# Optimization experiments

Hardware: AMD Instinct MI355X
Metric: run time of the kernel (lower is better)

## Reference

```python
import jax, jax.numpy as jnp
import numpy as np

D_MODEL = 2048
NHEAD = 16
HEAD_DIM = D_MODEL // NHEAD  # 128
B, S = 2, 2048
THETA = 10000.0


def setup_inputs() -> dict:
    key = jax.random.key(0)
    ks = jax.random.split(key, 10)
    sc = 1.0 / np.sqrt(D_MODEL)
    inp = {
        "x": jax.random.normal(ks[0], (B, S, D_MODEL), dtype=jnp.float32),
        "mask": jnp.tril(jnp.ones((1, 1, S, S), dtype=jnp.int32)),
        "Wq": jax.random.normal(ks[1], (D_MODEL, D_MODEL), dtype=jnp.float32) * sc,
        "bq": jax.random.normal(ks[2], (D_MODEL,), dtype=jnp.float32) * 0.01,
        "Wk": jax.random.normal(ks[3], (D_MODEL, D_MODEL), dtype=jnp.float32) * sc,
        "bk": jax.random.normal(ks[4], (D_MODEL,), dtype=jnp.float32) * 0.01,
        "Wv": jax.random.normal(ks[5], (D_MODEL, D_MODEL), dtype=jnp.float32) * sc,
        "bv": jax.random.normal(ks[6], (D_MODEL,), dtype=jnp.float32) * 0.01,
        "Wo": jax.random.normal(ks[7], (D_MODEL, D_MODEL), dtype=jnp.float32) * sc,
        "bo": jax.random.normal(ks[8], (D_MODEL,), dtype=jnp.float32) * 0.01,
    }
    return inp


def _rope(x):
    # x: [B, H, S, D]; rotary applied to first D/2 dims (per the torch module's chunk(2)).
    D = x.shape[-1]
    half = D // 2            # rotary slice size (64)
    quarter = half // 2      # rotate_half split (32)
    seq = x.shape[2]
    inv_freq = 1.0 / (THETA ** (jnp.arange(0, D, 2, dtype=jnp.float32) / D))  # [D/2]
    t = jnp.arange(seq, dtype=jnp.float32)
    freqs = jnp.einsum("i,j->ij", t, inv_freq)  # [S, D/2]
    # emb = cat(freqs, freqs) then sliced to [:half] == freqs[:, :half]
    cos = jnp.cos(freqs)[None, None, :, :half]  # [1,1,S,half]
    sin = jnp.sin(freqs)[None, None, :, :half]
    x_rope, x_pass = x[..., :half], x[..., half:]
    x1, x2 = x_rope[..., :quarter], x_rope[..., quarter:]
    rotated = jnp.concatenate([-x2, x1], axis=-1)
    x_rope = x_rope * cos + rotated * sin
    return jnp.concatenate([x_rope, x_pass], axis=-1)


def reference(x, mask, Wq, bq, Wk, bk, Wv, bv, Wo, bo):
    b, s, _ = x.shape
    def proj(W, bias):
        y = jnp.einsum("bsd,ed->bse", x, W) + bias  # torch Linear: x @ W.T + b
        return y.reshape(b, s, NHEAD, HEAD_DIM).transpose(0, 2, 1, 3)  # [B,H,S,Dh]
    q = _rope(proj(Wq, bq))
    k = _rope(proj(Wk, bk))
    v = proj(Wv, bv)
    scores = jnp.einsum("bhqd,bhkd->bhqk", q, k) / jnp.sqrt(jnp.float32(HEAD_DIM))
    scores = jnp.where(mask == 0, jnp.float32(-1e9), scores)
    a = jax.nn.softmax(scores, axis=-1)
    o = jnp.einsum("bhqk,bhkd->bhqd", a, v)
    o = o.transpose(0, 2, 1, 3).reshape(b, s, D_MODEL)
    return jnp.einsum("bsd,ed->bse", o, Wo) + bo
```

## Files before the change

kernel.cpp:

```cpp
#include <hip/hip_runtime.h>
#include <stdint.h>
#include <math.h>

typedef short short8 __attribute__((ext_vector_type(8)));
typedef float f32x4 __attribute__((ext_vector_type(4)));

#define S_LEN   2048
#define DMODEL  2048
#define NHEADS  16
#define HDIM    128
#define NBATCH  2
#define BHTOT   32
#define MROWS   4096

#define XB_OFF   ((size_t)0)
#define WQ_OFF   ((size_t)16777216)
#define WK_OFF   ((size_t)25165824)
#define WV_OFF   ((size_t)33554432)
#define Q_OFF    ((size_t)41943040)
#define K_OFF    ((size_t)58720256)
#define VT_OFF   ((size_t)75497472)
#define COS_OFF  ((size_t)92274688)
#define SIN_OFF  ((size_t)92798976)

__device__ __forceinline__ unsigned short f2bf(float f) {
  unsigned int u = __float_as_uint(f);
  unsigned int r = (u + 0x7FFFu + ((u >> 16) & 1u)) >> 16;
  return (unsigned short)r;
}
__device__ __forceinline__ float bf2f(unsigned short b) {
  return __uint_as_float(((unsigned int)b) << 16);
}

__device__ __forceinline__ void gl_lds16(const unsigned short* g, unsigned short* l) {
  __builtin_amdgcn_global_load_lds(
      (const __attribute__((address_space(1))) unsigned int*)(g),
      (__attribute__((address_space(3))) unsigned int*)(l),
      16, 0, 0);
}

__global__ __launch_bounds__(256) void k_cvt(const float* __restrict__ src,
                                             unsigned short* __restrict__ dst, int n4) {
  int i = blockIdx.x * 256 + threadIdx.x;
  if (i >= n4) return;
  float4 v = ((const float4*)src)[i];
  ushort4 o;
  o.x = f2bf(v.x); o.y = f2bf(v.y); o.z = f2bf(v.z); o.w = f2bf(v.w);
  ((ushort4*)dst)[i] = o;
}

__global__ __launch_bounds__(256) void k_prep(
    const float* __restrict__ x, const float* __restrict__ Wq,
    const float* __restrict__ Wk, const float* __restrict__ Wv,
    unsigned short* __restrict__ xb, unsigned short* __restrict__ wqb,
    unsigned short* __restrict__ wkb, unsigned short* __restrict__ wvb,
    float* __restrict__ ct, float* __restrict__ st) {
  int i = blockIdx.x * 256 + threadIdx.x;
  if (i < 5242880) {
    const float* s; unsigned short* d; int off;
    if (i < 2097152) { s = x; d = xb; off = i; }
    else {
      int j = i - 2097152, sel = j >> 20;
      off = j & 1048575;
      s = (sel == 0) ? Wq : (sel == 1 ? Wk : Wv);
      d = (sel == 0) ? wqb : (sel == 1 ? wkb : wvb);
    }
    float4 v = ((const float4*)s)[off];
    ushort4 o;
    o.x = f2bf(v.x); o.y = f2bf(v.y); o.z = f2bf(v.z); o.w = f2bf(v.w);
    ((ushort4*)d)[off] = o;
  } else {
    int j = i - 5242880;
    if (j < S_LEN * 64) {
      int s = j >> 6, jj = j & 63;
      float inv = expf(-(float)(2 * jj) * (9.210340371976184f / 128.0f));
      float ang = (float)s * inv;
      ct[j] = cosf(ang);
      st[j] = sinf(ang);
    }
  }
}

#define CP 136
__global__ __launch_bounds__(256) void k_gemm_qkv(
    const unsigned short* __restrict__ xb,
    const unsigned short* __restrict__ wqb, const unsigned short* __restrict__ wkb,
    const unsigned short* __restrict__ wvb,
    const float* __restrict__ bq, const float* __restrict__ bk, const float* __restrict__ bv,
    const float* __restrict__ ct, const float* __restrict__ st,
    unsigned short* __restrict__ qr, unsigned short* __restrict__ kr,
    unsigned short* __restrict__ vt) {
  __shared__ unsigned short SMEM[128 * CP];
  unsigned short* As = SMEM;
  unsigned short* Bs = SMEM + 8192;
  int bid = blockIdx.y * 32 + blockIdx.x;
  int nb = (bid & 7) * 192 + (bid >> 3);
  int m0 = (nb & 31) * 128;
  int n0g = (nb >> 5) * 128;
  int wsel = n0g >> 11;
  int nw0 = n0g & (DMODEL - 1);
  const unsigned short* W = (wsel == 0) ? wqb : (wsel == 1 ? wkb : wvb);
  const float* bias = (wsel == 0) ? bq : (wsel == 1 ? bk : bv);
  int tid = threadIdx.x, lane = tid & 63, wid = tid >> 6;
  int wr = wid >> 1, wc = wid & 1;
  int lq = lane & 15, lk = lane >> 4;
  int gr = wid * 32 + (lane >> 3);
  int gc = ((lane & 7) * 8) ^ ((lane >> 3) << 3);

  f32x4 acc[4][4];
#pragma unroll
  for (int m = 0; m < 4; m++)
#pragma unroll
    for (int n = 0; n < 4; n++) { acc[m][n][0]=0.f; acc[m][n][1]=0.f; acc[m][n][2]=0.f; acc[m][n][3]=0.f; }

  for (int k0 = 0; k0 < DMODEL; k0 += 64) {
#pragma unroll
    for (int i = 0; i < 4; i++) {
      gl_lds16(xb + (size_t)(m0 + gr + i * 8) * DMODEL + k0 + gc, As + (wid * 32 + i * 8) * 64);
      gl_lds16(W  + (size_t)(nw0 + gr + i * 8) * DMODEL + k0 + gc, Bs + (wid * 32 + i * 8) * 64);
    }
    __syncthreads();
#pragma unroll
    for (int kk = 0; kk < 2; kk++) {
      short8 af[4], bfr[4];
      int sw = (lq & 7) << 3;
#pragma unroll
      for (int m = 0; m < 4; m++)
        af[m] = *(const short8*)&As[(wr * 64 + m * 16 + lq) * 64 + ((kk * 32 + lk * 8) ^ sw)];
#pragma unroll
      for (int n = 0; n < 4; n++)
        bfr[n] = *(const short8*)&Bs[(wc * 64 + n * 16 + lq) * 64 + ((kk * 32 + lk * 8) ^ sw)];
#pragma unroll
      for (int m = 0; m < 4; m++)
#pragma unroll
        for (int n = 0; n < 4; n++)
          acc[m][n] = __builtin_amdgcn_mfma_f32_16x16x32_bf16(af[m], bfr[n], acc[m][n], 0, 0, 0);
    }
    __syncthreads();
  }

  int h = nw0 >> 7, b = m0 >> 11, s0 = m0 & (S_LEN - 1);
  float bi[4];
#pragma unroll
  for (int n = 0; n < 4; n++) bi[n] = bias[nw0 + wc * 64 + n * 16 + lq];

  if (wsel < 2) {
    float qs = (wsel == 0) ? 0.08838834764831843f : 1.0f;
    if (wc == 0) {
#pragma unroll
      for (int m = 0; m < 4; m++) {
        int sl = wr * 64 + m * 16 + lk * 4;
#pragma unroll
        for (int r = 0; r < 4; r++) {
          int s = (s0 + sl + r);
          const float* cb = ct + s * 64;
          const float* sb = st + s * 64;
#pragma unroll
          for (int n = 0; n < 2; n++) {
            int fq = n * 16 + lq;
            float x1 = acc[m][n][r] + bi[n];
            float x2 = acc[m][n + 2][r] + bi[n + 2];
            SMEM[(sl + r) * CP + fq]      = f2bf((x1 * cb[fq]      - x2 * sb[fq])      * qs);
            SMEM[(sl + r) * CP + fq + 32] = f2bf((x2 * cb[fq + 32] + x1 * sb[fq + 32]) * qs);
          }
        }
      }
    } else {
#pragma unroll
      for (int m = 0; m < 4; m++) {
        int sl = wr * 64 + m * 16 + lk * 4;
#pragma unroll
        for (int n = 0; n < 4; n++) {
          int fq = 64 + n * 16 + lq;
#pragma unroll
          for (int r = 0; r < 4; r++)
            SMEM[(sl + r) * CP + fq] = f2bf((acc[m][n][r] + bi[n]) * qs);
        }
      }
    }
    __syncthreads();
    int row = tid >> 1, hf2 = tid & 1;
    unsigned short* dstb = (wsel == 0 ? qr : kr) +
        ((size_t)(b * NHEADS + h) * S_LEN + s0 + row) * HDIM + hf2 * 64;
    const unsigned short* srcb = &SMEM[row * CP + hf2 * 64];
#pragma unroll
    for (int j = 0; j < 8; j++)
      *(short8*)(dstb + j * 8) = *(const short8*)(srcb + j * 8);
  } else {
#pragma unroll
    for (int m = 0; m < 4; m++) {
      int sl = wr * 64 + m * 16 + lk * 4;
#pragma unroll
      for (int n = 0; n < 4; n++) {
        int fq = wc * 64 + n * 16 + lq;
#pragma unroll
        for (int r = 0; r < 4; r++)
          SMEM[fq * CP + sl + r] = f2bf(acc[m][n][r] + bi[n]);
      }
    }
    __syncthreads();
    int row = tid >> 1, hf2 = tid & 1;
    unsigned short* dstb = vt +
        ((size_t)(b * NHEADS + h) * HDIM + row) * S_LEN + s0 + hf2 * 64;
    const unsigned short* srcb = &SMEM[row * CP + hf2 * 64];
#pragma unroll
    for (int j = 0; j < 8; j++)
      *(short8*)(dstb + j * 8) = *(const short8*)(srcb + j * 8);
  }
}

__device__ __forceinline__ void attn_sm_pv(
    f32x4* sacc, f32x4* acco, float* rm, float* rs,
    unsigned short (*Psw)[72], const unsigned short* V0,
    int lq, int lk, int rsw) {
  float mx4[4];
  int need = 0;
#pragma unroll
  for (int r = 0; r < 4; r++) {
    float mx = fmaxf(fmaxf(sacc[0][r], sacc[1][r]), fmaxf(sacc[2][r], sacc[3][r]));
    mx = fmaxf(mx, __shfl_xor(mx, 1, 64));
    mx = fmaxf(mx, __shfl_xor(mx, 2, 64));
    mx = fmaxf(mx, __shfl_xor(mx, 4, 64));
    mx = fmaxf(mx, __shfl_xor(mx, 8, 64));
    mx4[r] = mx;
    need |= (mx - rm[r] > 8.0f) ? 1 : 0;
  }
  if (__any(need)) {
#pragma unroll
    for (int r = 0; r < 4; r++) {
      float mnew = fmaxf(rm[r], mx4[r]);
      float corr = __expf(rm[r] - mnew);
      rs[r] *= corr;
#pragma unroll
      for (int nd = 0; nd < 8; nd++) acco[nd][r] *= corr;
      rm[r] = mnew;
    }
  }
#pragma unroll
  for (int r = 0; r < 4; r++) {
    float psum = 0.f;
#pragma unroll
    for (int n = 0; n < 4; n++) {
      float p = __expf(sacc[n][r] - rm[r]);
      sacc[n][r] = p;
      psum += p;
    }
    psum += __shfl_xor(psum, 1, 64);
    psum += __shfl_xor(psum, 2, 64);
    psum += __shfl_xor(psum, 4, 64);
    psum += __shfl_xor(psum, 8, 64);
    rs[r] += psum;
  }
#pragma unroll
  for (int n = 0; n < 4; n++)
#pragma unroll
    for (int r = 0; r < 4; r++)
      Psw[lk * 4 + r][n * 16 + lq] = f2bf(sacc[n][r]);
#pragma unroll
  for (int ks2 = 0; ks2 < 2; ks2++) {
    short8 pa = *(const short8*)&Psw[lq][ks2 * 32 + lk * 8];
#pragma unroll
    for (int nd = 0; nd < 8; nd++) {
      short8 vf = *(const short8*)&V0[(nd * 16 + lq) * 64 + ((ks2 * 32 + lk * 8) ^ rsw)];
      acco[nd] = __builtin_amdgcn_mfma_f32_16x16x32_bf16(pa, vf, acco[nd], 0, 0, 0);
    }
  }
}

__global__ __launch_bounds__(256, 2) void k_attn(
    const unsigned short* __restrict__ qr, const unsigned short* __restrict__ kr,
    const unsigned short* __restrict__ vt, unsigned short* __restrict__ ob) {
  __shared__ unsigned short Kl[2][64 * 128];
  __shared__ unsigned short Vl[2][128 * 64];
  __shared__ unsigned short Ps[4][16][72];
  int bh = blockIdx.x;
  int yy = blockIdx.y;
  int f = (yy < 8) ? yy : 23 - yy;
  int qtA = 31 - f, qtB = f;
  int q0A = qtA * 64, q0B = qtB * 64;
  int b = bh >> 4, h = bh & 15;
  int tid = threadIdx.x, lane = tid & 63, w = tid >> 6;
  int lq = lane & 15, lk = lane >> 4;
  const unsigned short* kbh = kr + (size_t)bh * S_LEN * HDIM;
  const unsigned short* vbh = vt + (size_t)bh * HDIM * S_LEN;
  int ksrow = tid >> 4;
  int kscol = ((tid & 15) * 8) ^ ((ksrow & 7) << 3);
  int vsrow = tid >> 3;
  int vscol = ((tid & 7) * 8) ^ ((vsrow & 7) << 3);
  int ldso = tid * 8;
  int rsw = (lq & 7) << 3;

  const unsigned short* qbA =
      qr + ((size_t)bh * S_LEN + q0A + w * 16 + lq) * HDIM + lk * 8;
  const unsigned short* qbB =
      qr + ((size_t)bh * S_LEN + q0B + w * 16 + lq) * HDIM + lk * 8;
  short8 qfA[4], qfB[4];
#pragma unroll
  for (int ks = 0; ks < 4; ks++) {
    qfA[ks] = *(const short8*)(qbA + ks * 32);
    qfB[ks] = *(const short8*)(qbB + ks * 32);
  }

  f32x4 accoA[8], accoB[8];
#pragma unroll
  for (int nd = 0; nd < 8; nd++) {
    accoA[nd][0]=0.f; accoA[nd][1]=0.f; accoA[nd][2]=0.f; accoA[nd][3]=0.f;
    accoB[nd][0]=0.f; accoB[nd][1]=0.f; accoB[nd][2]=0.f; accoB[nd][3]=0.f;
  }
  float rmA[4], rsA[4], rmB[4], rsB[4];
#pragma unroll
  for (int r = 0; r < 4; r++) { rmA[r] = -3.0e38f; rsA[r] = 0.f; rmB[r] = -3.0e38f; rsB[r] = 0.f; }

#pragma unroll
  for (int c = 0; c < 4; c++) {
    gl_lds16(kbh + (size_t)(c * 16 + ksrow) * HDIM + kscol, &Kl[0][c * 2048 + ldso]);
    gl_lds16(vbh + (size_t)(c * 32 + vsrow) * S_LEN + vscol, &Vl[0][c * 2048 + ldso]);
  }
  __syncthreads();
  int cur = 0;

  for (int t = 0; t <= qtA; t++) {
    int kv0 = t * 64;
    if (t < qtA) {
      int nx = kv0 + 64;
#pragma unroll
      for (int c = 0; c < 4; c++) {
        gl_lds16(kbh + (size_t)(nx + c * 16 + ksrow) * HDIM + kscol,
                 &Kl[cur ^ 1][c * 2048 + ldso]);
        gl_lds16(vbh + (size_t)(c * 32 + vsrow) * S_LEN + nx + vscol,
                 &Vl[cur ^ 1][c * 2048 + ldso]);
      }
    }
    const unsigned short* K0 = &Kl[cur][0];
    const unsigned short* V0 = &Vl[cur][0];
    bool actB = (t <= qtB);

    f32x4 saccA[4], saccB[4];
#pragma unroll
    for (int n = 0; n < 4; n++) {
      saccA[n][0]=0.f; saccA[n][1]=0.f; saccA[n][2]=0.f; saccA[n][3]=0.f;
      saccB[n][0]=0.f; saccB[n][1]=0.f; saccB[n][2]=0.f; saccB[n][3]=0.f;
    }
    if (actB) {
#pragma unroll
      for (int ks = 0; ks < 4; ks++)
#pragma unroll
        for (int n = 0; n < 4; n++) {
          short8 kf = *(const short8*)&K0[(n * 16 + lq) * 128 + ((ks * 32 + lk * 8) ^ rsw)];
          saccA[n] = __builtin_amdgcn_mfma_f32_16x16x32_bf16(qfA[ks], kf, saccA[n], 0, 0, 0);
          saccB[n] = __builtin_amdgcn_mfma_f32_16x16x32_bf16(qfB[ks], kf, saccB[n], 0, 0, 0);
        }
    } else {
#pragma unroll
      for (int ks = 0; ks < 4; ks++)
#pragma unroll
        for (int n = 0; n < 4; n++) {
          short8 kf = *(const short8*)&K0[(n * 16 + lq) * 128 + ((ks * 32 + lk * 8) ^ rsw)];
          saccA[n] = __builtin_amdgcn_mfma_f32_16x16x32_bf16(qfA[ks], kf, saccA[n], 0, 0, 0);
        }
    }
    if (t == qtA) {
#pragma unroll
      for (int n = 0; n < 4; n++)
#pragma unroll
        for (int r = 0; r < 4; r++) {
          int qrow = q0A + w * 16 + lk * 4 + r;
          int kvc = kv0 + n * 16 + lq;
          if (kvc > qrow) saccA[n][r] = -3.0e38f;
        }
    }
    attn_sm_pv(saccA, accoA, rmA, rsA, Ps[w], V0, lq, lk, rsw);
    if (actB) {
      if (t == qtB) {
#pragma unroll
        for (int n = 0; n < 4; n++)
#pragma unroll
          for (int r = 0; r < 4; r++) {
            int qrow = q0B + w * 16 + lk * 4 + r;
            int kvc = kv0 + n * 16 + lq;
            if (kvc > qrow) saccB[n][r] = -3.0e38f;
          }
      }
      attn_sm_pv(saccB, accoB, rmB, rsB, Ps[w], V0, lq, lk, rsw);
    }
    __syncthreads();
    cur ^= 1;
  }

#pragma unroll
  for (int r = 0; r < 4; r++) {
    float invA = 1.0f / rsA[r];
    int srowA = q0A + w * 16 + lk * 4 + r;
    unsigned short* dstA = ob + ((size_t)b * S_LEN + srowA) * DMODEL + h * HDIM;
#pragma unroll
    for (int nd = 0; nd < 8; nd++) dstA[nd * 16 + lq] = f2bf(accoA[nd][r] * invA);
    float invB = 1.0f / rsB[r];
    int srowB = q0B + w * 16 + lk * 4 + r;
    unsigned short* dstB = ob + ((size_t)b * S_LEN + srowB) * DMODEL + h * HDIM;
#pragma unroll
    for (int nd = 0; nd < 8; nd++) dstB[nd * 16 + lq] = f2bf(accoB[nd][r] * invB);
  }
}

__global__ __launch_bounds__(256) void k_gemm_out(
    const unsigned short* __restrict__ ob, const unsigned short* __restrict__ wob,
    const float* __restrict__ bo, float* __restrict__ out) {
  __shared__ unsigned short As[128][64];
  __shared__ unsigned short Bs[128][64];
  int bid = blockIdx.y * 32 + blockIdx.x;
  int nb = (bid & 7) * 64 + (bid >> 3);
  int m0 = (nb & 31) * 128;
  int n0 = (nb >> 5) * 128;
  int tid = threadIdx.x, lane = tid & 63, wid = tid >> 6;
  int wr = wid >> 1, wc = wid & 1;
  int lq = lane & 15, lk = lane >> 4;
  int gr = wid * 32 + (lane >> 3);
  int gc = ((lane & 7) * 8) ^ ((lane >> 3) << 3);

  f32x4 acc[4][4];
#pragma unroll
  for (int m = 0; m < 4; m++)
#pragma unroll
    for (int n = 0; n < 4; n++) { acc[m][n][0]=0.f; acc[m][n][1]=0.f; acc[m][n][2]=0.f; acc[m][n][3]=0.f; }

  for (int k0 = 0; k0 < DMODEL; k0 += 64) {
#pragma unroll
    for (int i = 0; i < 4; i++) {
      gl_lds16(ob  + (size_t)(m0 + gr + i * 8) * DMODEL + k0 + gc, &As[wid * 32 + i * 8][0]);
      gl_lds16(wob + (size_t)(n0 + gr + i * 8) * DMODEL + k0 + gc, &Bs[wid * 32 + i * 8][0]);
    }
    __syncthreads();
#pragma unroll
    for (int kk = 0; kk < 2; kk++) {
      short8 af[4], bfr[4];
      int sw = (lq & 7) << 3;
#pragma unroll
      for (int m = 0; m < 4; m++)
        af[m] = *(const short8*)&As[wr * 64 + m * 16 + lq][(kk * 32 + lk * 8) ^ sw];
#pragma unroll
      for (int n = 0; n < 4; n++)
        bfr[n] = *(const short8*)&Bs[wc * 64 + n * 16 + lq][(kk * 32 + lk * 8) ^ sw];
#pragma unroll
      for (int m = 0; m < 4; m++)
#pragma unroll
        for (int n = 0; n < 4; n++)
          acc[m][n] = __builtin_amdgcn_mfma_f32_16x16x32_bf16(af[m], bfr[n], acc[m][n], 0, 0, 0);
    }
    __syncthreads();
  }
#pragma unroll
  for (int n = 0; n < 4; n++) {
    int el = n0 + wc * 64 + n * 16 + lq;
    float bi = bo[el];
#pragma unroll
    for (int m = 0; m < 4; m++) {
      int row = m0 + wr * 64 + m * 16 + lk * 4;
#pragma unroll
      for (int r = 0; r < 4; r++)
        out[(size_t)(row + r) * DMODEL + el] = acc[m][n][r] + bi;
    }
  }
}

extern "C" void kernel_launch(void* const* d_in, const int* in_sizes, int n_in,
                              void* d_out, int out_size, void* d_ws, size_t ws_size,
                              hipStream_t stream) {
  const float* x  = (const float*)d_in[0];
  const float* Wq = (const float*)d_in[2];
  const float* bq = (const float*)d_in[3];
  const float* Wk = (const float*)d_in[4];
  const float* bk = (const float*)d_in[5];
  const float* Wv = (const float*)d_in[6];
  const float* bv = (const float*)d_in[7];
  const float* Wo = (const float*)d_in[8];
  const float* bo = (const float*)d_in[9];
  float* out = (float*)d_out;
  char* ws = (char*)d_ws;

  unsigned short* xb  = (unsigned short*)(ws + XB_OFF);
  unsigned short* wqb = (unsigned short*)(ws + WQ_OFF);
  unsigned short* wkb = (unsigned short*)(ws + WK_OFF);
  unsigned short* wvb = (unsigned short*)(ws + WV_OFF);
  unsigned short* qr  = (unsigned short*)(ws + Q_OFF);
  unsigned short* kr  = (unsigned short*)(ws + K_OFF);
  unsigned short* vt  = (unsigned short*)(ws + VT_OFF);
  float* ct = (float*)(ws + COS_OFF);
  float* st = (float*)(ws + SIN_OFF);

  k_prep<<<20992, 256, 0, stream>>>(x, Wq, Wk, Wv, xb, wqb, wkb, wvb, ct, st);
  k_gemm_qkv<<<dim3(MROWS / 128, 6144 / 128), 256, 0, stream>>>(
      xb, wqb, wkb, wvb, bq, bk, bv, ct, st, qr, kr, vt);
  k_cvt<<<(DMODEL * DMODEL / 4 + 255) / 256, 256, 0, stream>>>(Wo, wqb, DMODEL * DMODEL / 4);
  k_attn<<<dim3(BHTOT, 16), 256, 0, stream>>>(qr, kr, vt, xb);
  k_gemm_out<<<dim3(MROWS / 128, DMODEL / 128), 256, 0, stream>>>(xb, wqb, bo, out);
}
```

Before: 275.0 us.

## Fold Wo conversion into prep kernel, defer row-sum reduction, drop block swizzle

When the workspace is large enough, the Wo fp32-to-bf16 conversion moves into the prep kernel, writing to a dedicated workspace slot and removing the separate conversion launch. The attention softmax now keeps per-lane partial row sums and does the cross-lane shuffle reduction once at the end instead of every KV tile, cutting shuffle work in the inner loop. Both GEMMs also drop their grouped block-index swizzle in favour of a plain blockIdx mapping, which may hurt L2 reuse.

Result: faster. 259.3 us (-5.7%).

```diff
diff --git a/kernel.cpp b/kernel.cpp
--- a/kernel.cpp
+++ b/kernel.cpp
@@ -22,6 +22,8 @@
 #define VT_OFF   ((size_t)75497472)
 #define COS_OFF  ((size_t)92274688)
 #define SIN_OFF  ((size_t)92798976)
+#define WO_OFF   ((size_t)93323264)
+#define WS_NEED  (WO_OFF + (size_t)8388608)
 
 __device__ __forceinline__ unsigned short f2bf(float f) {
   unsigned int u = __float_as_uint(f);
@@ -52,25 +54,32 @@
 __global__ __launch_bounds__(256) void k_prep(
     const float* __restrict__ x, const float* __restrict__ Wq,
     const float* __restrict__ Wk, const float* __restrict__ Wv,
+    const float* __restrict__ Wo,
     unsigned short* __restrict__ xb, unsigned short* __restrict__ wqb,
     unsigned short* __restrict__ wkb, unsigned short* __restrict__ wvb,
+    unsigned short* __restrict__ wob,
     float* __restrict__ ct, float* __restrict__ st) {
   int i = blockIdx.x * 256 + threadIdx.x;
-  if (i < 5242880) {
+  if (i < 6291456) {
     const float* s; unsigned short* d; int off;
     if (i < 2097152) { s = x; d = xb; off = i; }
     else {
       int j = i - 2097152, sel = j >> 20;
       off = j & 1048575;
-      s = (sel == 0) ? Wq : (sel == 1 ? Wk : Wv);
-      d = (sel == 0) ? wqb : (sel == 1 ? wkb : wvb);
+      if (sel == 3) {
+        if (!wob) return;
+        s = Wo; d = wob;
+      } else {
+        s = (sel == 0) ? Wq : (sel == 1 ? Wk : Wv);
+        d = (sel == 0) ? wqb : (sel == 1 ? wkb : wvb);
+      }
     }
     float4 v = ((const float4*)s)[off];
     ushort4 o;
     o.x = f2bf(v.x); o.y = f2bf(v.y); o.z = f2bf(v.z); o.w = f2bf(v.w);
     ((ushort4*)d)[off] = o;
   } else {
-    int j = i - 5242880;
+    int j = i - 6291456;
     if (j < S_LEN * 64) {
       int s = j >> 6, jj = j & 63;
       float inv = expf(-(float)(2 * jj) * (9.210340371976184f / 128.0f));
@@ -93,10 +102,8 @@
   __shared__ unsigned short SMEM[128 * CP];
   unsigned short* As = SMEM;
   unsigned short* Bs = SMEM + 8192;
-  int bid = blockIdx.y * 32 + blockIdx.x;
-  int nb = (bid & 7) * 192 + (bid >> 3);
-  int m0 = (nb & 31) * 128;
-  int n0g = (nb >> 5) * 128;
+  int m0 = blockIdx.x * 128;
+  int n0g = blockIdx.y * 128;
   int wsel = n0g >> 11;
   int nw0 = n0g & (DMODEL - 1);
   const unsigned short* W = (wsel == 0) ? wqb : (wsel == 1 ? wkb : wvb);
@@ -245,10 +252,6 @@
       sacc[n][r] = p;
       psum += p;
     }
-    psum += __shfl_xor(psum, 1, 64);
-    psum += __shfl_xor(psum, 2, 64);
-    psum += __shfl_xor(psum, 4, 64);
-    psum += __shfl_xor(psum, 8, 64);
     rs[r] += psum;
   }
 #pragma unroll
@@ -389,12 +392,22 @@
 
 #pragma unroll
   for (int r = 0; r < 4; r++) {
-    float invA = 1.0f / rsA[r];
+    float sA = rsA[r];
+    sA += __shfl_xor(sA, 1, 64);
+    sA += __shfl_xor(sA, 2, 64);
+    sA += __shfl_xor(sA, 4, 64);
+    sA += __shfl_xor(sA, 8, 64);
+    float invA = 1.0f / sA;
     int srowA = q0A + w * 16 + lk * 4 + r;
     unsigned short* dstA = ob + ((size_t)b * S_LEN + srowA) * DMODEL + h * HDIM;
 #pragma unroll
     for (int nd = 0; nd < 8; nd++) dstA[nd * 16 + lq] = f2bf(accoA[nd][r] * invA);
-    float invB = 1.0f / rsB[r];
+    float sB = rsB[r];
+    sB += __shfl_xor(sB, 1, 64);
+    sB += __shfl_xor(sB, 2, 64);
+    sB += __shfl_xor(sB, 4, 64);
+    sB += __shfl_xor(sB, 8, 64);
+    float invB = 1.0f / sB;
     int srowB = q0B + w * 16 + lk * 4 + r;
     unsigned short* dstB = ob + ((size_t)b * S_LEN + srowB) * DMODEL + h * HDIM;
 #pragma unroll
@@ -407,10 +420,7 @@
     const float* __restrict__ bo, float* __restrict__ out) {
   __shared__ unsigned short As[128][64];
   __shared__ unsigned short Bs[128][64];
-  int bid = blockIdx.y * 32 + blockIdx.x;
-  int nb = (bid & 7) * 64 + (bid >> 3);
-  int m0 = (nb & 31) * 128;
-  int n0 = (nb >> 5) * 128;
+  int m0 = blockIdx.x * 128, n0 = blockIdx.y * 128;
   int tid = threadIdx.x, lane = tid & 63, wid = tid >> 6;
   int wr = wid >> 1, wc = wid & 1;
   int lq = lane & 15, lk = lane >> 4;
@@ -486,11 +496,15 @@
   unsigned short* vt  = (unsigned short*)(ws + VT_OFF);
   float* ct = (float*)(ws + COS_OFF);
   float* st = (float*)(ws + SIN_OFF);
-
-  k_prep<<<20992, 256, 0, stream>>>(x, Wq, Wk, Wv, xb, wqb, wkb, wvb, ct, st);
+  bool haveWo = (ws_size >= WS_NEED);
+  unsigned short* wob = haveWo ? (unsigned short*)(ws + WO_OFF) : nullptr;
+
+  k_prep<<<25088, 256, 0, stream>>>(x, Wq, Wk, Wv, Wo, xb, wqb, wkb, wvb, wob, ct, st);
   k_gemm_qkv<<<dim3(MROWS / 128, 6144 / 128), 256, 0, stream>>>(
       xb, wqb, wkb, wvb, bq, bk, bv, ct, st, qr, kr, vt);
-  k_cvt<<<(DMODEL * DMODEL / 4 + 255) / 256, 256, 0, stream>>>(Wo, wqb, DMODEL * DMODEL / 4);
+  if (!haveWo)
+    k_cvt<<<(DMODEL * DMODEL / 4 + 255) / 256, 256, 0, stream>>>(Wo, wqb, DMODEL * DMODEL / 4);
   k_attn<<<dim3(BHTOT, 16), 256, 0, stream>>>(qr, kr, vt, xb);
-  k_gemm_out<<<dim3(MROWS / 128, DMODEL / 128), 256, 0, stream>>>(xb, wqb, bo, out);
-}
+  k_gemm_out<<<dim3(MROWS / 128, DMODEL / 128), 256, 0, stream>>>(
+      xb, haveWo ? wob : wqb, bo, out);
+}
```
